# Performance work log

Measured on AMD Instinct MI355X. Metric: run time of the kernel, lower is better.

## Reference

```python
import jax, jax.numpy as jnp
import numpy as np

N_NODES = 100000
N_EDGES = 1600000
D_IN = 128
D_OUT = 128


def setup_inputs() -> dict:
    key = jax.random.key(0)
    k1, k2, k3, k4, k5 = jax.random.split(key, 5)
    x = jax.random.normal(k1, (N_NODES, D_IN), dtype=jnp.float32)
    x_0 = jax.random.normal(k2, (N_NODES, D_IN), dtype=jnp.float32)
    edge_index = jax.random.randint(k3, (2, N_EDGES), 0, N_NODES, dtype=jnp.int64)
    # GCNConv linear weight (glorot-ish scale) and bias
    W = jax.random.normal(k4, (D_IN, D_OUT), dtype=jnp.float32) / np.sqrt(D_IN)
    b = jax.random.normal(k5, (D_OUT,), dtype=jnp.float32) * 0.01
    return {"x": x, "x_0": x_0, "W": W, "b": b, "edge_index": edge_index}


def reference(x, x_0, W, b, edge_index):
    # SemiGCNConv.forward: relu(GCNConv(x, edge_index)); x_0 is unused.
    N = x.shape[0]
    # GCNConv default: add self-loops, symmetric normalization
    loop = jnp.arange(N, dtype=edge_index.dtype)
    src = jnp.concatenate([edge_index[0], loop])  # [E+N]
    dst = jnp.concatenate([edge_index[1], loop])  # [E+N]
    # degree of target nodes (edge_weight = 1)
    deg = jax.ops.segment_sum(jnp.ones_like(dst, dtype=x.dtype), dst, num_segments=N)
    deg_inv_sqrt = jnp.where(deg > 0, jax.lax.rsqrt(deg), 0.0)
    norm = deg_inv_sqrt[src] * deg_inv_sqrt[dst]  # [E+N]
    # linear transform first (PyG order), then normalized scatter-add aggregation
    h = x @ W  # [N, D_OUT]
    msg = h[src] * norm[:, None]  # gather + scale, [E+N, D_OUT]
    out = jax.ops.segment_sum(msg, dst, num_segments=N) + b
    return jax.nn.relu(out)
```

## Files before the change

kernel.cpp:

```cpp
#include <hip/hip_runtime.h>

#define N_NODES 100000
#define N_EDGES 1600000
#define D 128
#define G 64
#define NB 1563
#define NB_PAD 1568
#define CAP 1536
#define EPT 16

typedef __attribute__((ext_vector_type(8))) short bf16x8;
typedef __attribute__((ext_vector_type(4))) float f32x4;

__device__ inline float bf2f(unsigned short u) {
    return __uint_as_float(((unsigned int)u) << 16);
}
__device__ inline unsigned short f2bf(float f) {
    unsigned int u = __float_as_uint(f);
    unsigned int r = u + 0x7FFF + ((u >> 16) & 1);
    return (unsigned short)(r >> 16);
}

__device__ inline int wave_incl_scan(int v, int lane) {
    #pragma unroll
    for (int off = 1; off < 64; off <<= 1) {
        int y = __shfl_up(v, off);
        if (lane >= off) v += y;
    }
    return v;
}

__global__ __launch_bounds__(256) void bin_count(const int* __restrict__ ei,
                                                 int* __restrict__ deg,
                                                 int* __restrict__ gcursor,
                                                 unsigned int* __restrict__ bins) {
    __shared__ int hist[NB];
    __shared__ int base[NB];
    const int tid = threadIdx.x;
    for (int i = tid; i < NB; i += 256) hist[i] = 0;
    __syncthreads();

    const long long e0 = (long long)blockIdx.x * (256 * EPT) + (long long)tid * EPT;
    const bool active = (e0 < N_EDGES);
    unsigned int packed[EPT]; int bkt[EPT]; int rnk[EPT];
    if (active) {
        const int4* s4 = (const int4*)(ei + e0);
        const int4* d4 = (const int4*)(ei + N_EDGES + e0);
        #pragma unroll
        for (int q = 0; q < EPT / 4; ++q) {
            int4 s = s4[q], d = d4[q];
            int j = q * 4;
            bkt[j+0] = d.x >> 6; packed[j+0] = (unsigned)s.x | ((unsigned)(d.x & 63) << 17);
            bkt[j+1] = d.y >> 6; packed[j+1] = (unsigned)s.y | ((unsigned)(d.y & 63) << 17);
            bkt[j+2] = d.z >> 6; packed[j+2] = (unsigned)s.z | ((unsigned)(d.z & 63) << 17);
            bkt[j+3] = d.w >> 6; packed[j+3] = (unsigned)s.w | ((unsigned)(d.w & 63) << 17);
            atomicAdd(&deg[d.x], 1);
            atomicAdd(&deg[d.y], 1);
            atomicAdd(&deg[d.z], 1);
            atomicAdd(&deg[d.w], 1);
        }
        #pragma unroll
        for (int j = 0; j < EPT; ++j) rnk[j] = atomicAdd(&hist[bkt[j]], 1);
    }
    __syncthreads();
    for (int i = tid; i < NB; i += 256) {
        int c = hist[i];
        base[i] = c ? atomicAdd(&gcursor[i], c) : 0;
    }
    __syncthreads();
    if (active) {
        #pragma unroll
        for (int j = 0; j < EPT; ++j) {
            int pos = base[bkt[j]] + rnk[j];
            if (pos < CAP) bins[(size_t)bkt[j] * CAP + pos] = packed[j];
        }
    }
}

__global__ __launch_bounds__(512) void gemm_h_mfma(
        const float* __restrict__ x, const float* __restrict__ W,
        const int* __restrict__ deg, unsigned short* __restrict__ h) {
    __shared__ unsigned short wt[D * D];
    const int tid  = threadIdx.x;
    const int lane = tid & 63;
    const int wv   = tid >> 6;
    const int rb   = blockIdx.x * 128 + wv * 16;

    int arow = rb + (lane & 15);
    if (arow >= N_NODES) arow = N_NODES - 1;
    const float4* xrow = (const float4*)(x + (size_t)arow * D);
    float4 af[8];
    #pragma unroll
    for (int kt = 0; kt < 4; ++kt) {
        int fi = kt * 8 + (lane >> 4) * 2;
        af[kt * 2]     = xrow[fi];
        af[kt * 2 + 1] = xrow[fi + 1];
    }

    const float4* W4 = (const float4*)W;
    float4 wreg[8];
    #pragma unroll
    for (int i = 0; i < 8; ++i) wreg[i] = W4[tid + 512 * i];
    #pragma unroll
    for (int i = 0; i < 8; ++i) {
        int idx = tid + 512 * i;
        int k  = idx >> 5;
        int c0 = (idx & 31) * 4;
        float v[4] = {wreg[i].x, wreg[i].y, wreg[i].z, wreg[i].w};
        #pragma unroll
        for (int j = 0; j < 4; ++j) {
            int c = c0 + j;
            int byte = (c * 256 + k * 2) ^ ((c & 7) << 4);
            *(unsigned short*)((char*)wt + byte) = f2bf(v[j]);
        }
    }
    __syncthreads();

    bf16x8 a[4];
    #pragma unroll
    for (int kt = 0; kt < 4; ++kt) {
        float4 u = af[kt * 2], v = af[kt * 2 + 1];
        a[kt][0] = (short)f2bf(u.x); a[kt][1] = (short)f2bf(u.y);
        a[kt][2] = (short)f2bf(u.z); a[kt][3] = (short)f2bf(u.w);
        a[kt][4] = (short)f2bf(v.x); a[kt][5] = (short)f2bf(v.y);
        a[kt][6] = (short)f2bf(v.z); a[kt][7] = (short)f2bf(v.w);
    }

    f32x4 acc[8];
    #pragma unroll
    for (int ct = 0; ct < 8; ++ct) acc[ct] = (f32x4){0.f, 0.f, 0.f, 0.f};

    const int cbase = lane & 15;
    const int kgrp  = (lane >> 4) * 8;
    #pragma unroll
    for (int ct = 0; ct < 8; ++ct) {
        int c = ct * 16 + cbase;
        #pragma unroll
        for (int kt = 0; kt < 4; ++kt) {
            int byte = (c * 256 + (kt * 32 + kgrp) * 2) ^ ((c & 7) << 4);
            bf16x8 bfr = *(const bf16x8*)((const char*)wt + byte);
            acc[ct] = __builtin_amdgcn_mfma_f32_16x16x32_bf16(a[kt], bfr, acc[ct], 0, 0, 0);
        }
    }

    float dq[4]; int orow[4];
    #pragma unroll
    for (int q = 0; q < 4; ++q) {
        orow[q] = rb + (lane >> 4) * 4 + q;
        int rr = orow[q] < N_NODES ? orow[q] : 0;
        dq[q] = rsqrtf((float)deg[rr] + 1.0f);
    }
    #pragma unroll
    for (int ct = 0; ct < 8; ++ct) {
        int col = ct * 16 + (lane & 15);
        #pragma unroll
        for (int q = 0; q < 4; ++q) {
            if (orow[q] < N_NODES)
                h[(size_t)orow[q] * D + col] = f2bf(acc[ct][q] * dq[q]);
        }
    }
}

__global__ __launch_bounds__(256) void bucket_gather(const unsigned int* __restrict__ bins,
                                                     const int* __restrict__ gcursor,
                                                     const ushort4* __restrict__ h4,
                                                     const float4* __restrict__ b4,
                                                     float4* __restrict__ out4) {
    __shared__ int degL[G];
    __shared__ int rsL[G];
    __shared__ int curL[G];
    __shared__ int csrL[CAP];
    const int b = blockIdx.x, t = threadIdx.x;
    int cb = gcursor[b];
    if (cb > CAP) cb = CAP;
    if (t < G) { degL[t] = 0; curL[t] = 0; }
    __syncthreads();
    const unsigned int* mybins = bins + (size_t)b * CAP;
    for (int i = t; i < cb; i += 256)
        atomicAdd(&degL[(mybins[i] >> 17) & 63], 1);
    __syncthreads();
    if (t < G) {
        int v = degL[t];
        int incl = wave_incl_scan(v, t);
        rsL[t] = incl - v;
    }
    __syncthreads();
    for (int i = t; i < cb; i += 256) {
        unsigned int u = mybins[i];
        int dl = (u >> 17) & 63;
        int pos = rsL[dl] + atomicAdd(&curL[dl], 1);
        csrL[pos] = (int)(u & 0x1FFFF);
    }
    __syncthreads();

    const int c = t & 31, g = t >> 5;
    for (int nl = g; nl < G; nl += 8) {
        int node = b * G + nl;
        if (node >= N_NODES) break;
        int rs = rsL[nl], dg = degL[nl];
        ushort4 hv = h4[(size_t)node * 32 + c];
        float4 acc = {bf2f(hv.x), bf2f(hv.y), bf2f(hv.z), bf2f(hv.w)};
        int j = 0;
        for (; j + 4 <= dg; j += 4) {
            int s0 = csrL[rs + j], s1 = csrL[rs + j + 1];
            int s2 = csrL[rs + j + 2], s3 = csrL[rs + j + 3];
            ushort4 v0 = h4[(size_t)s0 * 32 + c];
            ushort4 v1 = h4[(size_t)s1 * 32 + c];
            ushort4 v2 = h4[(size_t)s2 * 32 + c];
            ushort4 v3 = h4[(size_t)s3 * 32 + c];
            acc.x += bf2f(v0.x) + bf2f(v1.x) + bf2f(v2.x) + bf2f(v3.x);
            acc.y += bf2f(v0.y) + bf2f(v1.y) + bf2f(v2.y) + bf2f(v3.y);
            acc.z += bf2f(v0.z) + bf2f(v1.z) + bf2f(v2.z) + bf2f(v3.z);
            acc.w += bf2f(v0.w) + bf2f(v1.w) + bf2f(v2.w) + bf2f(v3.w);
        }
        for (; j < dg; ++j) {
            int s = csrL[rs + j];
            ushort4 v = h4[(size_t)s * 32 + c];
            acc.x += bf2f(v.x); acc.y += bf2f(v.y);
            acc.z += bf2f(v.z); acc.w += bf2f(v.w);
        }
        float dn = rsqrtf((float)dg + 1.0f);
        float4 bb = b4[c];
        float4 o;
        o.x = fmaxf(fmaf(dn, acc.x, bb.x), 0.f);
        o.y = fmaxf(fmaf(dn, acc.y, bb.y), 0.f);
        o.z = fmaxf(fmaf(dn, acc.z, bb.z), 0.f);
        o.w = fmaxf(fmaf(dn, acc.w, bb.w), 0.f);
        out4[(size_t)node * 32 + c] = o;
    }
}

extern "C" void kernel_launch(void* const* d_in, const int* in_sizes, int n_in,
                              void* d_out, int out_size, void* d_ws, size_t ws_size,
                              hipStream_t stream) {
    const float* x  = (const float*)d_in[0];
    const float* W  = (const float*)d_in[2];
    const float* b  = (const float*)d_in[3];
    const int*   ei = (const int*)d_in[4];
    float* out = (float*)d_out;

    unsigned short* h  = (unsigned short*)d_ws;
    int*   deg         = (int*)(h + (size_t)N_NODES * D);
    int*   gcursor     = deg + N_NODES;
    unsigned int* bins = (unsigned int*)(gcursor + NB_PAD);

    hipMemsetAsync(deg, 0, (N_NODES + NB_PAD) * sizeof(int), stream);

    bin_count<<<(N_EDGES + 256 * EPT - 1) / (256 * EPT), 256, 0, stream>>>(ei, deg, gcursor, bins);
    gemm_h_mfma<<<(N_NODES + 127) / 128, 512, 0, stream>>>(x, W, deg, h);
    bucket_gather<<<NB, 256, 0, stream>>>(bins, gcursor, (const ushort4*)h,
                                          (const float4*)b, (float4*)out);
}
```

Before: 294.9 us.

## Use coarser 256-node buckets and compute degrees from bins instead of global atomics

Bucket width grows from 64 to 256 destination nodes, so there are fewer bins and the binning kernel does fewer global cursor atomics, with fewer edges per thread. The global per-edge degree atomics are removed; a new kernel counts degrees per bucket in shared memory from the binned edges. The gather kernel launches four blocks per bucket, and each block filters the bucket's edges for its 64-node quarter, so every block now reads the full bucket. This adds one kernel launch and redundant bin reads, and a quarter holding more than SUBCAP edges would be silently dropped.

```diff
diff --git a/kernel.cpp b/kernel.cpp
--- a/kernel.cpp
+++ b/kernel.cpp
@@ -3,11 +3,12 @@
 #define N_NODES 100000
 #define N_EDGES 1600000
 #define D 128
-#define G 64
-#define NB 1563
-#define NB_PAD 1568
-#define CAP 1536
-#define EPT 16
+#define G 256
+#define NB 391
+#define NB_PAD 392
+#define CAP 6144
+#define SUBCAP 1536
+#define EPT 4
 
 typedef __attribute__((ext_vector_type(8))) short bf16x8;
 typedef __attribute__((ext_vector_type(4))) float f32x4;
@@ -31,7 +32,6 @@
 }
 
 __global__ __launch_bounds__(256) void bin_count(const int* __restrict__ ei,
-                                                 int* __restrict__ deg,
                                                  int* __restrict__ gcursor,
                                                  unsigned int* __restrict__ bins) {
     __shared__ int hist[NB];
@@ -44,21 +44,12 @@
     const bool active = (e0 < N_EDGES);
     unsigned int packed[EPT]; int bkt[EPT]; int rnk[EPT];
     if (active) {
-        const int4* s4 = (const int4*)(ei + e0);
-        const int4* d4 = (const int4*)(ei + N_EDGES + e0);
-        #pragma unroll
-        for (int q = 0; q < EPT / 4; ++q) {
-            int4 s = s4[q], d = d4[q];
-            int j = q * 4;
-            bkt[j+0] = d.x >> 6; packed[j+0] = (unsigned)s.x | ((unsigned)(d.x & 63) << 17);
-            bkt[j+1] = d.y >> 6; packed[j+1] = (unsigned)s.y | ((unsigned)(d.y & 63) << 17);
-            bkt[j+2] = d.z >> 6; packed[j+2] = (unsigned)s.z | ((unsigned)(d.z & 63) << 17);
-            bkt[j+3] = d.w >> 6; packed[j+3] = (unsigned)s.w | ((unsigned)(d.w & 63) << 17);
-            atomicAdd(&deg[d.x], 1);
-            atomicAdd(&deg[d.y], 1);
-            atomicAdd(&deg[d.z], 1);
-            atomicAdd(&deg[d.w], 1);
-        }
+        int4 s = *(const int4*)(ei + e0);
+        int4 d = *(const int4*)(ei + N_EDGES + e0);
+        bkt[0] = d.x >> 8; packed[0] = (unsigned)s.x | ((unsigned)(d.x & 255) << 17);
+        bkt[1] = d.y >> 8; packed[1] = (unsigned)s.y | ((unsigned)(d.y & 255) << 17);
+        bkt[2] = d.z >> 8; packed[2] = (unsigned)s.z | ((unsigned)(d.z & 255) << 17);
+        bkt[3] = d.w >> 8; packed[3] = (unsigned)s.w | ((unsigned)(d.w & 255) << 17);
         #pragma unroll
         for (int j = 0; j < EPT; ++j) rnk[j] = atomicAdd(&hist[bkt[j]], 1);
     }
@@ -75,6 +66,23 @@
             if (pos < CAP) bins[(size_t)bkt[j] * CAP + pos] = packed[j];
         }
     }
+}
+
+__global__ __launch_bounds__(256) void deg_bins(const unsigned int* __restrict__ bins,
+                                                const int* __restrict__ gcursor,
+                                                int* __restrict__ deg) {
+    __shared__ int degL[G];
+    const int b = blockIdx.x, t = threadIdx.x;
+    degL[t] = 0;
+    __syncthreads();
+    int cb = gcursor[b];
+    if (cb > CAP) cb = CAP;
+    const unsigned int* mybins = bins + (size_t)b * CAP;
+    for (int i = t; i < cb; i += 256)
+        atomicAdd(&degL[(mybins[i] >> 17) & 255], 1);
+    __syncthreads();
+    int node = b * G + t;
+    if (node < N_NODES) deg[node] = degL[t];
 }
 
 __global__ __launch_bounds__(512) void gemm_h_mfma(
@@ -166,20 +174,24 @@
                                                      const ushort4* __restrict__ h4,
                                                      const float4* __restrict__ b4,
                                                      float4* __restrict__ out4) {
-    __shared__ int degL[G];
-    __shared__ int rsL[G];
-    __shared__ int curL[G];
-    __shared__ int csrL[CAP];
-    const int b = blockIdx.x, t = threadIdx.x;
+    __shared__ int degL[64];
+    __shared__ int rsL[64];
+    __shared__ int curL[64];
+    __shared__ int csrL[SUBCAP];
+    const int j = blockIdx.x, t = threadIdx.x;
+    const int b = j >> 2, q = j & 3;
     int cb = gcursor[b];
     if (cb > CAP) cb = CAP;
-    if (t < G) { degL[t] = 0; curL[t] = 0; }
+    if (t < 64) { degL[t] = 0; curL[t] = 0; }
     __syncthreads();
     const unsigned int* mybins = bins + (size_t)b * CAP;
-    for (int i = t; i < cb; i += 256)
-        atomicAdd(&degL[(mybins[i] >> 17) & 63], 1);
-    __syncthreads();
-    if (t < G) {
+    for (int i = t; i < cb; i += 256) {
+        unsigned int u = mybins[i];
+        if (((u >> 23) & 3) == (unsigned)q)
+            atomicAdd(&degL[(u >> 17) & 63], 1);
+    }
+    __syncthreads();
+    if (t < 64) {
         int v = degL[t];
         int incl = wave_incl_scan(v, t);
         rsL[t] = incl - v;
@@ -187,23 +199,25 @@
     __syncthreads();
     for (int i = t; i < cb; i += 256) {
         unsigned int u = mybins[i];
-        int dl = (u >> 17) & 63;
-        int pos = rsL[dl] + atomicAdd(&curL[dl], 1);
-        csrL[pos] = (int)(u & 0x1FFFF);
+        if (((u >> 23) & 3) == (unsigned)q) {
+            int dl = (u >> 17) & 63;
+            int pos = rsL[dl] + atomicAdd(&curL[dl], 1);
+            if (pos < SUBCAP) csrL[pos] = (int)(u & 0x1FFFF);
+        }
     }
     __syncthreads();
 
     const int c = t & 31, g = t >> 5;
-    for (int nl = g; nl < G; nl += 8) {
-        int node = b * G + nl;
+    for (int nl = g; nl < 64; nl += 8) {
+        int node = j * 64 + nl;
         if (node >= N_NODES) break;
         int rs = rsL[nl], dg = degL[nl];
         ushort4 hv = h4[(size_t)node * 32 + c];
         float4 acc = {bf2f(hv.x), bf2f(hv.y), bf2f(hv.z), bf2f(hv.w)};
-        int j = 0;
-        for (; j + 4 <= dg; j += 4) {
-            int s0 = csrL[rs + j], s1 = csrL[rs + j + 1];
-            int s2 = csrL[rs + j + 2], s3 = csrL[rs + j + 3];
+        int jj = 0;
+        for (; jj + 4 <= dg; jj += 4) {
+            int s0 = csrL[rs + jj],     s1 = csrL[rs + jj + 1];
+            int s2 = csrL[rs + jj + 2], s3 = csrL[rs + jj + 3];
             ushort4 v0 = h4[(size_t)s0 * 32 + c];
             ushort4 v1 = h4[(size_t)s1 * 32 + c];
             ushort4 v2 = h4[(size_t)s2 * 32 + c];
@@ -213,8 +227,8 @@
             acc.z += bf2f(v0.z) + bf2f(v1.z) + bf2f(v2.z) + bf2f(v3.z);
             acc.w += bf2f(v0.w) + bf2f(v1.w) + bf2f(v2.w) + bf2f(v3.w);
         }
-        for (; j < dg; ++j) {
-            int s = csrL[rs + j];
+        for (; jj < dg; ++jj) {
+            int s = csrL[rs + jj];
             ushort4 v = h4[(size_t)s * 32 + c];
             acc.x += bf2f(v.x); acc.y += bf2f(v.y);
             acc.z += bf2f(v.z); acc.w += bf2f(v.w);
@@ -244,10 +258,11 @@
     int*   gcursor     = deg + N_NODES;
     unsigned int* bins = (unsigned int*)(gcursor + NB_PAD);
 
-    hipMemsetAsync(deg, 0, (N_NODES + NB_PAD) * sizeof(int), stream);
-
-    bin_count<<<(N_EDGES + 256 * EPT - 1) / (256 * EPT), 256, 0, stream>>>(ei, deg, gcursor, bins);
+    hipMemsetAsync(gcursor, 0, NB_PAD * sizeof(int), stream);
+
+    bin_count<<<(N_EDGES + 256 * EPT - 1) / (256 * EPT), 256, 0, stream>>>(ei, gcursor, bins);
+    deg_bins<<<NB, 256, 0, stream>>>(bins, gcursor, deg);
     gemm_h_mfma<<<(N_NODES + 127) / 128, 512, 0, stream>>>(x, W, deg, h);
-    bucket_gather<<<NB, 256, 0, stream>>>(bins, gcursor, (const ushort4*)h,
-                                          (const float4*)b, (float4*)out);
-}
+    bucket_gather<<<NB * 4, 256, 0, stream>>>(bins, gcursor, (const ushort4*)h,
+                                              (const float4*)b, (float4*)out);
+}
```

New measurement: 283.3 us. 4.0% less time.
